# Kernel optimization log

Measured on AMD Instinct MI355X. Metric: run time of the kernel, lower is better.

Reference implementation:

```python
import jax, jax.numpy as jnp
import numpy as np

WS = 7            # window size (49 tokens per window)
NH = 6            # heads
LOG100 = 4.605170185988092  # clamp max for logit_scale, = log(100)
EPS = 1e-12       # F.normalize eps


def setup_inputs() -> dict:
    key = jax.random.key(0)
    ks = jax.random.split(key, 6)
    B, H, W, C = 32, 64, 64, 60
    x = jax.random.normal(ks[0], (B, H, W, C), dtype=jnp.float32)
    qkv_w = jax.random.normal(ks[1], (3 * C, C), dtype=jnp.float32) * 0.05
    qkv_b = jax.random.normal(ks[2], (3 * C,), dtype=jnp.float32) * 0.05
    logit_scale = jax.random.normal(ks[3], (NH, 1, 1), dtype=jnp.float32)
    proj_w = jax.random.normal(ks[4], (C, C), dtype=jnp.float32) * 0.05
    proj_b = jax.random.normal(ks[5], (C,), dtype=jnp.float32) * 0.05
    return {"x": x, "qkv_w": qkv_w, "qkv_b": qkv_b,
            "logit_scale": logit_scale, "proj_w": proj_w, "proj_b": proj_b}


def reference(x, qkv_w, qkv_b, logit_scale, proj_w, proj_b):
    B, H, W, C = x.shape
    hd = C // NH
    pad = (-H) % WS  # 64 -> 70 needs pad 6 (same for W)
    Hp, Wp = H + pad, W + pad
    nw = Hp // WS
    # pad bottom/right then window-partition: [B,Hp,Wp,C] -> [B*nw*nw, 49, C]
    xp = jnp.pad(x, ((0, 0), (0, pad), (0, pad), (0, 0)))
    xw = xp.reshape(B, nw, WS, nw, WS, C).transpose(0, 1, 3, 2, 4, 5)
    xw = xw.reshape(B * nw * nw, WS * WS, C)
    # qkv projection -> [3, nW, NH, 49, hd]
    qkv = (xw @ qkv_w.T + qkv_b).reshape(-1, WS * WS, 3, NH, hd)
    qkv = qkv.transpose(2, 0, 3, 1, 4)
    q, k, v = qkv[0], qkv[1], qkv[2]
    # cosine attention: L2-normalize q,k (clamped norm), exp-clamped logit scale
    qn = q / jnp.maximum(jnp.linalg.norm(q, axis=-1, keepdims=True), EPS)
    kn = k / jnp.maximum(jnp.linalg.norm(k, axis=-1, keepdims=True), EPS)
    scale = jnp.exp(jnp.minimum(logit_scale, LOG100))  # [NH,1,1]
    attn = jnp.einsum('whqd,whkd->whqk', qn, kn) * scale
    a = jax.nn.softmax(attn, axis=-1)
    out = jnp.einsum('whqk,whkd->whqd', a, v)  # [nW,NH,49,hd]
    out = out.transpose(0, 2, 1, 3).reshape(-1, WS * WS, C)
    out = out @ proj_w.T + proj_b
    # window reverse + unpad -> [B,H,W,C]
    out = out.reshape(B, nw, nw, WS, WS, C).transpose(0, 1, 3, 2, 4, 5)
    out = out.reshape(B, Hp, Wp, C)
    return out[:, :H, :W, :]
```

## Files before the change

### kernel.cpp

```cpp
#include <hip/hip_runtime.h>
#include <hip/hip_bf16.h>


#define WSZ 7
#define NT 49
#define CH 60
#define IMG 64
#define LOG100F 4.605170185988092f

__global__ __launch_bounds__(384, 5)
void swin_win_attn(const float* __restrict__ x,
                   const float* __restrict__ qkv_w,
                   const float* __restrict__ qkv_b,
                   const float* __restrict__ logit_scale,
                   const float* __restrict__ proj_w,
                   const float* __restrict__ proj_b,
                   float* __restrict__ out)
{
    __shared__ __align__(16) float s_x[NT * CH];
    __shared__ __align__(16) float s_q[6 * NT * 10];
    __shared__ __align__(16) float s_k[6 * NT * 12];
    __shared__ __align__(16) float s_v[6 * NT * 12];

    const int tid  = threadIdx.x;
    const int lane = tid & 63;
    const int wv   = __builtin_amdgcn_readfirstlane(tid >> 6);
    const int w  = blockIdx.x;
    const int b  = w / 100;
    const int wy = (w / 10) % 10;
    const int wx = w % 10;
    const int row0 = wy * WSZ;
    const int col0 = wx * WSZ;

    for (int idx = tid; idx < NT * 15; idx += 384) {
        int t = idx / 15, m = idx - t * 15;
        int r  = row0 + t / WSZ;
        int cc = col0 + t % WSZ;
        float4 v = make_float4(0.f, 0.f, 0.f, 0.f);
        if (r < IMG && cc < IMG)
            v = reinterpret_cast<const float4*>(x + ((b * IMG + r) * IMG + cc) * CH)[m];
        *reinterpret_cast<float4*>(s_x + t * CH + 4 * m) = v;
    }
    for (int idx = tid; idx < 2 * 6 * NT; idx += 384) {
        int r = idx >> 1, p = idx & 1;
        s_k[r * 12 + 10 + p] = 0.f;
        s_v[r * 12 + 10 + p] = 0.f;
    }
    __syncthreads();

    if (tid < 360) {
        const int c    = tid % 180;
        const int half = tid / 180;
        const int part = c / 60;
        const int cl   = c - 60 * part;
        const int h = cl / 10, d = cl - 10 * (cl / 10);
        float4 w4[15];
        const float4* wp = reinterpret_cast<const float4*>(qkv_w + c * CH);
        #pragma unroll
        for (int m = 0; m < 15; ++m) w4[m] = wp[m];
        const float bias = qkv_b[c];
        const int t0 = half ? 25 : 0, t1 = half ? NT : 25;
        for (int t = t0; t < t1; ++t) {
            float a = bias;
            const float4* xr = reinterpret_cast<const float4*>(s_x + t * CH);
            #pragma unroll
            for (int m = 0; m < 15; ++m) {
                float4 xv = xr[m];
                a += xv.x * w4[m].x + xv.y * w4[m].y + xv.z * w4[m].z + xv.w * w4[m].w;
            }
            if (part == 0)      s_q[(h * NT + t) * 10 + d] = a;
            else if (part == 1) s_k[(h * NT + t) * 12 + d] = a;
            else                s_v[(h * NT + t) * 12 + d] = a;
        }
    }
    __syncthreads();

    if (tid < 6 * NT) {
        float* p = s_k + tid * 12;
        float ss = 0.f;
        #pragma unroll
        for (int d = 0; d < 10; ++d) ss += p[d] * p[d];
        float inv = 1.f / fmaxf(sqrtf(ss), 1e-12f);
        #pragma unroll
        for (int d = 0; d < 10; ++d) p[d] *= inv;
    }
    __syncthreads();

    if (tid < 6 * NT) {
        const int h = tid / NT, i = tid - h * NT;
        float scale = __expf(fminf(logit_scale[h], LOG100F));
        float q[10];
        {
            const float2* qp = reinterpret_cast<const float2*>(s_q + tid * 10);
            #pragma unroll
            for (int d = 0; d < 5; ++d) { float2 t2 = qp[d]; q[2*d] = t2.x; q[2*d+1] = t2.y; }
            float ss = 0.f;
            #pragma unroll
            for (int d = 0; d < 10; ++d) ss += q[d] * q[d];
            float inv = scale / fmaxf(sqrtf(ss), 1e-12f);
            #pragma unroll
            for (int d = 0; d < 10; ++d) q[d] *= inv;
        }
        float a[NT];
        const float4* kb = reinterpret_cast<const float4*>(s_k + h * NT * 12);
        #pragma unroll
        for (int j = 0; j < NT; ++j) {
            float4 k0 = kb[j * 3 + 0];
            float4 k1 = kb[j * 3 + 1];
            float4 k2 = kb[j * 3 + 2];
            a[j] = q[0]*k0.x + q[1]*k0.y + q[2]*k0.z + q[3]*k0.w
                 + q[4]*k1.x + q[5]*k1.y + q[6]*k1.z + q[7]*k1.w
                 + q[8]*k2.x + q[9]*k2.y;
        }
        float m = a[0];
        #pragma unroll
        for (int j = 1; j < NT; ++j) m = fmaxf(m, a[j]);
        float s = 0.f;
        #pragma unroll
        for (int j = 0; j < NT; ++j) { float e = __expf(a[j] - m); a[j] = e; s += e; }
        float o[10];
        #pragma unroll
        for (int d = 0; d < 10; ++d) o[d] = 0.f;
        const float4* vb = reinterpret_cast<const float4*>(s_v + h * NT * 12);
        #pragma unroll
        for (int j = 0; j < NT; ++j) {
            float4 v0 = vb[j * 3 + 0];
            float4 v1 = vb[j * 3 + 1];
            float4 v2 = vb[j * 3 + 2];
            float aj = a[j];
            o[0] += aj * v0.x; o[1] += aj * v0.y; o[2] += aj * v0.z; o[3] += aj * v0.w;
            o[4] += aj * v1.x; o[5] += aj * v1.y; o[6] += aj * v1.z; o[7] += aj * v1.w;
            o[8] += aj * v2.x; o[9] += aj * v2.y;
        }
        float inv = 1.f / s;
        float* op = s_x + i * CH + h * 10;
        #pragma unroll
        for (int d = 0; d < 5; ++d)
            *reinterpret_cast<float2*>(op + 2 * d) =
                make_float2(o[2*d] * inv, o[2*d+1] * inv);
    }
    __syncthreads();

    if (lane < 60) {
        float4 w4[15];
        const float4* wp = reinterpret_cast<const float4*>(proj_w + lane * CH);
        #pragma unroll
        for (int m = 0; m < 15; ++m) w4[m] = wp[m];
        const float bias = proj_b[lane];
        for (int t = wv; t < NT; t += 6) {
            int r  = row0 + t / WSZ;
            int cc = col0 + t % WSZ;
            float a = bias;
            const float4* xr = reinterpret_cast<const float4*>(s_x + t * CH);
            #pragma unroll
            for (int m = 0; m < 15; ++m) {
                float4 xv = xr[m];
                a += xv.x * w4[m].x + xv.y * w4[m].y
                   + xv.z * w4[m].z + xv.w * w4[m].w;
            }
            if (r < IMG && cc < IMG)
                out[((b * IMG + r) * IMG + cc) * CH + lane] = a;
        }
    }
}

extern "C" void kernel_launch(void* const* d_in, const int* in_sizes, int n_in,
                              void* d_out, int out_size, void* d_ws, size_t ws_size,
                              hipStream_t stream) {
    hipLaunchKernelGGL(swin_win_attn, dim3(3200), dim3(384), 0, stream,
                       (const float*)d_in[0], (const float*)d_in[1],
                       (const float*)d_in[2], (const float*)d_in[3],
                       (const float*)d_in[4], (const float*)d_in[5],
                       (float*)d_out);
}
```

Measured before the change: 256.7 us.

## Drop x staging in LDS, use online softmax, reuse q buffer for output

The QKV projection now reads the input rows straight from global memory, which removes the shared-memory staging buffer and its barrier. Attention switches to a single-pass online softmax that only rescales when the running max grows by more than 8. This removes the 49-entry score array held in registers. The attention output is written back into the q buffer, and the output projection skips padded tokens. The aim is lower LDS and register use for better occupancy, at the cost of every lane issuing broadcast global loads of x, which may add memory latency.

After: 437.0 us. +70.2%, slower.

```diff
diff --git a/kernel.cpp b/kernel.cpp
--- a/kernel.cpp
+++ b/kernel.cpp
@@ -1,5 +1,4 @@
 #include <hip/hip_runtime.h>
-#include <hip/hip_bf16.h>
 
 
 #define WSZ 7
@@ -17,7 +16,6 @@
                    const float* __restrict__ proj_b,
                    float* __restrict__ out)
 {
-    __shared__ __align__(16) float s_x[NT * CH];
     __shared__ __align__(16) float s_q[6 * NT * 10];
     __shared__ __align__(16) float s_k[6 * NT * 12];
     __shared__ __align__(16) float s_v[6 * NT * 12];
@@ -32,22 +30,12 @@
     const int row0 = wy * WSZ;
     const int col0 = wx * WSZ;
 
-    for (int idx = tid; idx < NT * 15; idx += 384) {
-        int t = idx / 15, m = idx - t * 15;
-        int r  = row0 + t / WSZ;
-        int cc = col0 + t % WSZ;
-        float4 v = make_float4(0.f, 0.f, 0.f, 0.f);
-        if (r < IMG && cc < IMG)
-            v = reinterpret_cast<const float4*>(x + ((b * IMG + r) * IMG + cc) * CH)[m];
-        *reinterpret_cast<float4*>(s_x + t * CH + 4 * m) = v;
+    if (tid < 6 * NT) {
+        s_k[tid * 12 + 10] = 0.f;
+        s_k[tid * 12 + 11] = 0.f;
+        s_v[tid * 12 + 10] = 0.f;
+        s_v[tid * 12 + 11] = 0.f;
     }
-    for (int idx = tid; idx < 2 * 6 * NT; idx += 384) {
-        int r = idx >> 1, p = idx & 1;
-        s_k[r * 12 + 10 + p] = 0.f;
-        s_v[r * 12 + 10 + p] = 0.f;
-    }
-    __syncthreads();
-
     if (tid < 360) {
         const int c    = tid % 180;
         const int half = tid / 180;
@@ -61,12 +49,16 @@
         const float bias = qkv_b[c];
         const int t0 = half ? 25 : 0, t1 = half ? NT : 25;
         for (int t = t0; t < t1; ++t) {
+            const int tr = t / WSZ, tc = t - WSZ * tr;
             float a = bias;
-            const float4* xr = reinterpret_cast<const float4*>(s_x + t * CH);
-            #pragma unroll
-            for (int m = 0; m < 15; ++m) {
-                float4 xv = xr[m];
-                a += xv.x * w4[m].x + xv.y * w4[m].y + xv.z * w4[m].z + xv.w * w4[m].w;
+            if (row0 + tr < IMG && col0 + tc < IMG) {
+                const float4* xr = reinterpret_cast<const float4*>(
+                    x + ((b * IMG + row0 + tr) * IMG + col0 + tc) * CH);
+                #pragma unroll
+                for (int m = 0; m < 15; ++m) {
+                    float4 xv = xr[m];
+                    a += xv.x * w4[m].x + xv.y * w4[m].y + xv.z * w4[m].z + xv.w * w4[m].w;
+                }
             }
             if (part == 0)      s_q[(h * NT + t) * 10 + d] = a;
             else if (part == 1) s_k[(h * NT + t) * 12 + d] = a;
@@ -87,13 +79,13 @@
     __syncthreads();
 
     if (tid < 6 * NT) {
-        const int h = tid / NT, i = tid - h * NT;
+        const int h = tid / NT;
         float scale = __expf(fminf(logit_scale[h], LOG100F));
         float q[10];
         {
             const float2* qp = reinterpret_cast<const float2*>(s_q + tid * 10);
             #pragma unroll
-            for (int d = 0; d < 5; ++d) { float2 t2 = qp[d]; q[2*d] = t2.x; q[2*d+1] = t2.y; }
+            for (int d2 = 0; d2 < 5; ++d2) { float2 t2 = qp[d2]; q[2*d2] = t2.x; q[2*d2+1] = t2.y; }
             float ss = 0.f;
             #pragma unroll
             for (int d = 0; d < 10; ++d) ss += q[d] * q[d];
@@ -101,65 +93,71 @@
             #pragma unroll
             for (int d = 0; d < 10; ++d) q[d] *= inv;
         }
-        float a[NT];
+        float m = -1e30f, s = 0.f;
+        float o[10];
+        #pragma unroll
+        for (int d = 0; d < 10; ++d) o[d] = 0.f;
         const float4* kb = reinterpret_cast<const float4*>(s_k + h * NT * 12);
-        #pragma unroll
+        const float4* vb = reinterpret_cast<const float4*>(s_v + h * NT * 12);
         for (int j = 0; j < NT; ++j) {
             float4 k0 = kb[j * 3 + 0];
             float4 k1 = kb[j * 3 + 1];
             float4 k2 = kb[j * 3 + 2];
-            a[j] = q[0]*k0.x + q[1]*k0.y + q[2]*k0.z + q[3]*k0.w
-                 + q[4]*k1.x + q[5]*k1.y + q[6]*k1.z + q[7]*k1.w
-                 + q[8]*k2.x + q[9]*k2.y;
-        }
-        float m = a[0];
-        #pragma unroll
-        for (int j = 1; j < NT; ++j) m = fmaxf(m, a[j]);
-        float s = 0.f;
-        #pragma unroll
-        for (int j = 0; j < NT; ++j) { float e = __expf(a[j] - m); a[j] = e; s += e; }
-        float o[10];
-        #pragma unroll
-        for (int d = 0; d < 10; ++d) o[d] = 0.f;
-        const float4* vb = reinterpret_cast<const float4*>(s_v + h * NT * 12);
-        #pragma unroll
-        for (int j = 0; j < NT; ++j) {
+            float a = q[0]*k0.x + q[1]*k0.y + q[2]*k0.z + q[3]*k0.w
+                    + q[4]*k1.x + q[5]*k1.y + q[6]*k1.z + q[7]*k1.w
+                    + q[8]*k2.x + q[9]*k2.y;
+            if (a > m + 8.f) {
+                float r = __expf(m - a);
+                s *= r;
+                #pragma unroll
+                for (int d = 0; d < 10; ++d) o[d] *= r;
+                m = a;
+            }
+            float p = __expf(a - m);
+            s += p;
             float4 v0 = vb[j * 3 + 0];
             float4 v1 = vb[j * 3 + 1];
             float4 v2 = vb[j * 3 + 2];
-            float aj = a[j];
-            o[0] += aj * v0.x; o[1] += aj * v0.y; o[2] += aj * v0.z; o[3] += aj * v0.w;
-            o[4] += aj * v1.x; o[5] += aj * v1.y; o[6] += aj * v1.z; o[7] += aj * v1.w;
-            o[8] += aj * v2.x; o[9] += aj * v2.y;
+            o[0] += p * v0.x; o[1] += p * v0.y; o[2] += p * v0.z; o[3] += p * v0.w;
+            o[4] += p * v1.x; o[5] += p * v1.y; o[6] += p * v1.z; o[7] += p * v1.w;
+            o[8] += p * v2.x; o[9] += p * v2.y;
         }
-        float inv = 1.f / s;
-        float* op = s_x + i * CH + h * 10;
+        float invs = 1.f / s;
+        float* op = s_q + tid * 10;
         #pragma unroll
-        for (int d = 0; d < 5; ++d)
-            *reinterpret_cast<float2*>(op + 2 * d) =
-                make_float2(o[2*d] * inv, o[2*d+1] * inv);
+        for (int d2 = 0; d2 < 5; ++d2)
+            *reinterpret_cast<float2*>(op + 2 * d2) =
+                make_float2(o[2*d2] * invs, o[2*d2+1] * invs);
     }
     __syncthreads();
 
     if (lane < 60) {
-        float4 w4[15];
+        float wr[60];
         const float4* wp = reinterpret_cast<const float4*>(proj_w + lane * CH);
         #pragma unroll
-        for (int m = 0; m < 15; ++m) w4[m] = wp[m];
+        for (int m = 0; m < 15; ++m) {
+            float4 t4 = wp[m];
+            wr[4*m+0] = t4.x; wr[4*m+1] = t4.y; wr[4*m+2] = t4.z; wr[4*m+3] = t4.w;
+        }
         const float bias = proj_b[lane];
         for (int t = wv; t < NT; t += 6) {
-            int r  = row0 + t / WSZ;
-            int cc = col0 + t % WSZ;
-            float a = bias;
-            const float4* xr = reinterpret_cast<const float4*>(s_x + t * CH);
-            #pragma unroll
-            for (int m = 0; m < 15; ++m) {
-                float4 xv = xr[m];
-                a += xv.x * w4[m].x + xv.y * w4[m].y
-                   + xv.z * w4[m].z + xv.w * w4[m].w;
+            const int tr = t / WSZ, tc = t - WSZ * tr;
+            const int r  = row0 + tr;
+            const int cc = col0 + tc;
+            if (r < IMG && cc < IMG) {
+                float a = bias;
+                #pragma unroll
+                for (int h2 = 0; h2 < 6; ++h2) {
+                    const float2* orow = reinterpret_cast<const float2*>(s_q + (h2 * NT + t) * 10);
+                    #pragma unroll
+                    for (int m2 = 0; m2 < 5; ++m2) {
+                        float2 ov = orow[m2];
+                        a += ov.x * wr[h2 * 10 + 2 * m2]
+                           + ov.y * wr[h2 * 10 + 2 * m2 + 1];
+                    }
+                }
+                out[((b * IMG + r) * IMG + cc) * CH + lane] = a;
             }
-            if (r < IMG && cc < IMG)
-                out[((b * IMG + r) * IMG + cc) * CH + lane] = a;
         }
     }
 }
```
